# Kernel optimization log

Hardware: AMD Instinct MI355X
Metric: run time of the kernel (lower is better)

## Reference

```python
import jax, jax.numpy as jnp
import numpy as np

K = 16          # knn neighbors (init kwarg k)
GROUPS = 4      # GroupNorm groups
EPS = 1e-5
SLOPE = 0.2     # LeakyReLU negative slope


def fps(xyz, n):
    """Farthest point sampling. xyz: (B,N,3) -> idx (B,n). First index is 0 (pointnet2 convention)."""
    B, N, _ = xyz.shape

    def step(carry, _):
        dist, last = carry
        p = jnp.take_along_axis(xyz, last[:, None, None], axis=1)  # (B,1,3)
        d = jnp.sum((xyz - p) ** 2, axis=-1)                       # (B,N)
        dist = jnp.minimum(dist, d)
        nxt = jnp.argmax(dist, axis=-1).astype(jnp.int32)
        return (dist, nxt), nxt

    init = (jnp.full((B, N), jnp.inf, xyz.dtype), jnp.zeros((B,), jnp.int32))
    _, idxs = jax.lax.scan(step, init, None, length=n - 1)  # (n-1, B)
    return jnp.concatenate([jnp.zeros((B, 1), jnp.int32), idxs.T], axis=1)


def graph_feature(cq, fq, ck, fk):
    """DGCNN edge features. cq:(B,Q,3) fq:(B,Q,C) ck:(B,N,3) fk:(B,N,C) -> (B,Q,K,2C)."""
    d2 = (jnp.sum(cq * cq, -1)[:, :, None]
          - 2.0 * jnp.einsum('bqc,bnc->bqn', cq, ck)
          + jnp.sum(ck * ck, -1)[:, None, :])        # (B,Q,N)
    _, idx = jax.lax.top_k(-d2, K)                    # (B,Q,K) nearest first
    nb = jax.vmap(lambda f_, i_: f_[i_])(fk, idx)     # (B,Q,K,C)
    ctr = jnp.broadcast_to(fq[:, :, None, :], nb.shape)
    return jnp.concatenate([nb - ctr, ctr], axis=-1)


def conv_gn_lrelu(y, W, gw, gb):
    """1x1 Conv2d (no bias) + GroupNorm(4) + LeakyReLU(0.2). y: (B,Q,K,Cin), W: (Cout,Cin)."""
    y = jnp.einsum('bqkc,oc->bqko', y, W)
    B, Q, Kk, C = y.shape
    yg = y.reshape(B, Q * Kk, GROUPS, C // GROUPS)
    m = yg.mean(axis=(1, 3), keepdims=True)
    v = yg.var(axis=(1, 3), keepdims=True)
    y = ((yg - m) * jax.lax.rsqrt(v + EPS)).reshape(B, Q, Kk, C) * gw + gb
    return jnp.where(y > 0, y, SLOPE * y)


def setup_inputs() -> dict:
    key = jax.random.key(0)
    ks = jax.random.split(key, 16)
    B, N = 8, 4096
    s = lambda k_, shape, scale=0.1: (jax.random.normal(k_, shape, jnp.float32) * scale)
    return {
        'x': jax.random.normal(ks[0], (B, N, 7), jnp.float32),
        'W_in': s(ks[1], (8, 3), 0.5), 'b_in': s(ks[2], (8,), 0.02),
        'W1': s(ks[3], (32, 16), 0.2), 'g1w': jnp.ones((32,), jnp.float32), 'g1b': jnp.zeros((32,), jnp.float32),
        'W2': s(ks[4], (64, 64), 0.1), 'g2w': jnp.ones((64,), jnp.float32), 'g2b': jnp.zeros((64,), jnp.float32),
        'W3': s(ks[5], (64, 128), 0.1), 'g3w': jnp.ones((64,), jnp.float32), 'g3b': jnp.zeros((64,), jnp.float32),
        'W4': s(ks[6], (128, 128), 0.1), 'g4w': jnp.ones((128,), jnp.float32), 'g4b': jnp.zeros((128,), jnp.float32),
        'num0': 1024,
    }


def reference(x, W_in, b_in, W1, g1w, g1b, W2, g2w, g2b, W3, g3w, g3b, W4, g4w, g4b, num0):
    coor, normal, plane = x[..., :3], x[..., 3:6], x[..., 6:7]   # (B,N,3),(B,N,3),(B,N,1)

    # input_trans: Conv1d(3,8,1)
    f = jnp.einsum('bnc,oc->bno', coor, W_in) + b_in             # (B,N,8)

    g = graph_feature(coor, f, coor, f)                          # (B,N,K,16)
    f = conv_gn_lrelu(g, W1, g1w, g1b).max(axis=2)               # (B,N,32)

    idx = fps(coor, num0)
    gather = lambda a: jnp.take_along_axis(a, idx[:, :, None], axis=1)
    coor_q, normal_q, plane_q, f_q = gather(coor), gather(normal), gather(plane), gather(f)

    g = graph_feature(coor_q, f_q, coor, f)                      # (B,num0,K,64)
    f = conv_gn_lrelu(g, W2, g2w, g2b).max(axis=2)               # (B,num0,64)
    coor, normal, plane = coor_q, normal_q, plane_q

    g = graph_feature(coor, f, coor, f)                          # (B,num0,K,128)
    f = conv_gn_lrelu(g, W3, g3w, g3b).max(axis=2)               # (B,num0,64)

    idx = fps(coor, num0)  # source uses num[0] again
    gather = lambda a: jnp.take_along_axis(a, idx[:, :, None], axis=1)
    coor_q, normal_q, plane_q, f_q = gather(coor), gather(normal), gather(plane), gather(f)

    g = graph_feature(coor_q, f_q, coor, f)                      # (B,num0,K,128)
    f = conv_gn_lrelu(g, W4, g4w, g4b).max(axis=2)               # (B,num0,128)

    return coor_q, f, normal_q, plane_q
```

## Files before the change

### kernel.cpp

```cpp
#include <hip/hip_runtime.h>
#include <cstdint>

static constexpr int B   = 8;
static constexpr int N0  = 4096;
static constexpr int NQ  = 1024;
static constexpr int KNB = 16;

__device__ __forceinline__ unsigned long long wave_max_u64_l63(unsigned long long k) {
#define STEPU_(ctrl)                                                                    \
  {                                                                                     \
    unsigned lo_ = (unsigned)k, hi_ = (unsigned)(k >> 32);                              \
    unsigned plo_ = (unsigned)__builtin_amdgcn_update_dpp((int)lo_, (int)lo_, ctrl,     \
                                                          0xf, 0xf, false);             \
    unsigned phi_ = (unsigned)__builtin_amdgcn_update_dpp((int)hi_, (int)hi_, ctrl,     \
                                                          0xf, 0xf, false);             \
    unsigned long long pk_ = ((unsigned long long)phi_ << 32) | plo_;                   \
    if (pk_ > k) k = pk_;                                                               \
  }
  STEPU_(0x111) STEPU_(0x112) STEPU_(0x114) STEPU_(0x118) STEPU_(0x142) STEPU_(0x143)
#undef STEPU_
  return k;
}

__global__ void prep_kernel(const float* __restrict__ x,
                            const float* __restrict__ W_in,
                            const float* __restrict__ b_in,
                            float4* __restrict__ c4, float* __restrict__ nrm,
                            float* __restrict__ pl, float* __restrict__ f0) {
  int i = blockIdx.x * 256 + threadIdx.x;
  if (i >= B * N0) return;
  const float* xp = x + (size_t)i * 7;
  float cx = xp[0], cy = xp[1], cz = xp[2];
  float kk = __fadd_rn(__fadd_rn(__fmul_rn(cx, cx), __fmul_rn(cy, cy)), __fmul_rn(cz, cz));
  c4[i] = make_float4(cx, cy, cz, kk);
  nrm[i * 3 + 0] = xp[3]; nrm[i * 3 + 1] = xp[4]; nrm[i * 3 + 2] = xp[5];
  pl[i] = xp[6];
#pragma unroll
  for (int o = 0; o < 8; o++) {
    f0[(size_t)i * 8 + o] = cx * W_in[o * 3 + 0] + cy * W_in[o * 3 + 1] + cz * W_in[o * 3 + 2] + b_in[o];
  }
}

template <int NC>
__device__ __forceinline__ void knn_body(int bq, int lane,
                                         const float4* __restrict__ q4,
                                         const float4* __restrict__ k4,
                                         int Q, int Nk, int* __restrict__ out) {
  int b = bq / Q;
  float4 q = q4[bq];
  const float4* kb = k4 + (size_t)b * Nk + lane;
  const float INF    = __int_as_float(0x7f800000);
  const float NEGINF = __int_as_float(0xff800000);
  float myd = INF;
  int   myi = 0;
  float kth = INF;
  const bool isl0 = (lane & 15) == 0;
  constexpr int G = (NC >= 8) ? 8 : NC;
  for (int c0 = 0; c0 < NC; c0 += G) {
    float dg[G];
#pragma unroll
    for (int u = 0; u < G; u++) {
      float4 kp = kb[(c0 + u) * 64];
      float dot = __fadd_rn(__fadd_rn(__fmul_rn(q.x, kp.x), __fmul_rn(q.y, kp.y)),
                            __fmul_rn(q.z, kp.z));
      dg[u] = __fadd_rn(__fsub_rn(q.w, __fmul_rn(2.0f, dot)), kp.w);
    }
#pragma unroll
    for (int u = 0; u < G; u++) {
      float d = dg[u];
      unsigned long long m = __ballot(d < kth);
      while (m) {
        int j = __builtin_ctzll(m);
        float dv = __int_as_float(__builtin_amdgcn_readlane(__float_as_int(d), j));
        int   iv = (c0 + u) * 64 + j;
        bool gt = (myd > dv);
        float pd = __int_as_float(__builtin_amdgcn_update_dpp(
            0, __float_as_int(myd), 0x111, 0xf, 0xf, true));
        int   pi = __builtin_amdgcn_update_dpp(0, myi, 0x111, 0xf, 0xf, true);
        pd = isl0 ? NEGINF : pd;
        bool tp = (pd > dv);
        float nd = tp ? pd : dv;
        int   ni = tp ? pi : iv;
        myd = gt ? nd : myd;
        myi = gt ? ni : myi;
        kth = __int_as_float(__builtin_amdgcn_readlane(__float_as_int(myd), 15));
        m = __ballot(d < kth);
        m = (j < 63) ? (m & (~0ull << (j + 1))) : 0ull;
      }
    }
  }
  if (lane < KNB) out[(size_t)bq * KNB + lane] = myi;
}

template <int CF, int CO>
__device__ __forceinline__ void ctry_body(int i, int total, const float* __restrict__ fq,
                                          const float* __restrict__ W,
                                          float* __restrict__ ctrY,
                                          const int* __restrict__ ridx, int Q, int Nsrc) {
  if (i >= total) return;
  int o = i % CO, bq = i / CO;
  const float* fp;
  if (ridx) {
    int b = bq / Q;
    fp = fq + ((size_t)b * Nsrc + ridx[bq]) * CF;
  } else {
    fp = fq + (size_t)bq * CF;
  }
  const float* wp = W + (size_t)o * (2 * CF) + CF;
  float acc = 0.f;
#pragma unroll
  for (int c = 0; c < CF; c++) acc = fmaf(fp[c], wp[c], acc);
  ctrY[i] = acc;
}

template <int NPTS>
__device__ __forceinline__ void fps_body(const float4* __restrict__ cb, int* w) {
  constexpr int BLK = 256;
  constexpr int M = NPTS / BLK;
  constexpr int NW = BLK / 64;
  __shared__ __align__(16) float2 sxy[NPTS];
  __shared__ float szz[NPTS];
  __shared__ __align__(16) unsigned long long skey[2][NW];
  const int tid = threadIdx.x;
  const int wid = tid >> 6, lane = tid & 63;
  float cx[M], cy[M], cz[M], dist[M];
#pragma unroll
  for (int i = 0; i < M; i++) {
    float4 p = cb[tid * M + i];
    cx[i] = p.x; cy[i] = p.y; cz[i] = p.z;
    dist[i] = 3.4e38f;
    sxy[tid * M + i] = make_float2(p.x, p.y);
    szz[tid * M + i] = p.z;
  }
  w[0] = w[1] = w[2] = w[3] = 0;
  float4 p0 = cb[0];
  float px = p0.x, py = p0.y, pz = p0.z;
  __syncthreads();
  for (int t = 1; t < NQ; t++) {
    float bv = -1.f; int bi = 0;
#pragma unroll
    for (int i = 0; i < M; i++) {
      float dx = __fsub_rn(cx[i], px), dy = __fsub_rn(cy[i], py), dz = __fsub_rn(cz[i], pz);
      float d = __fadd_rn(__fadd_rn(__fmul_rn(dx, dx), __fmul_rn(dy, dy)), __fmul_rn(dz, dz));
      float dd = dist[i]; dd = (d < dd) ? d : dd; dist[i] = dd;
      if (dd > bv) { bv = dd; bi = tid * M + i; }
    }
    unsigned long long k =
        ((unsigned long long)__float_as_uint(bv) << 12) | (unsigned)(4095 - bi);
    k = wave_max_u64_l63(k);
    int p = t & 1;
    if (lane == 63) skey[p][wid] = k;
    __syncthreads();
    ulonglong2 ab = *(const ulonglong2*)&skey[p][0];
    ulonglong2 cd = *(const ulonglong2*)&skey[p][2];
    unsigned long long m0 = (ab.x > ab.y) ? ab.x : ab.y;
    unsigned long long m1 = (cd.x > cd.y) ? cd.x : cd.y;
    unsigned long long mk = (m0 > m1) ? m0 : m1;
    int win = 4095 - (int)(mk & 0xFFFull);
    float2 pxy = sxy[win];
    px = pxy.x; py = pxy.y; pz = szz[win];
    if (t == tid) w[0] = win;
    if (t == tid + 256) w[1] = win;
    if (t == tid + 512) w[2] = win;
    if (t == tid + 768) w[3] = win;
  }
}

template <int CF, int CO, int NT>
__device__ __forceinline__ void edgeconv_body(
    int blkid, const float* __restrict__ fq, const float* __restrict__ fk,
    const int* __restrict__ knn, const float* __restrict__ Wfull,
    const float* __restrict__ ctrY, const int* __restrict__ ridx,
    float* __restrict__ ymin, float* __restrict__ ymax,
    float* __restrict__ gstats, int Q, int Nk) {
  constexpr int J = CO / 4;
  constexpr int SEC = J * CF + 8;
  constexpr int NWARP = NT / 64;
  __shared__ float Wl[4 * SEC];
  __shared__ float sstat[8];
  for (int t = threadIdx.x; t < CO * CF; t += NT) {
    int o = t / CF, c = t % CF;
    Wl[(o / J) * SEC + (o % J) * CF + c] = Wfull[(size_t)o * (2 * CF) + c];
  }
  if (threadIdx.x < 8) sstat[threadIdx.x] = 0.0f;
  __syncthreads();
  const int wid = threadIdx.x >> 6, lane = threadIdx.x & 63;
  const int bq = blkid * NWARP + wid;
  const int b = bq / Q;
  const int g = lane >> 4, k = lane & 15;
  const int ni = knn[(size_t)bq * KNB + k];
  const float* nbp = fk + (size_t)(b * Nk + ni) * CF;
  const float* cp = ridx ? fq + ((size_t)b * Nk + ridx[bq]) * CF
                         : fq + (size_t)bq * CF;
  float acc[J];
#pragma unroll
  for (int j = 0; j < J; j++) acc[j] = 0.0f;
  const float* wg = &Wl[g * SEC];
#pragma unroll
  for (int c = 0; c < CF; c += 4) {
    float4 nb4 = *(const float4*)(nbp + c);
    float4 c4  = *(const float4*)(cp + c);
    float e0 = nb4.x - c4.x, e1 = nb4.y - c4.y, e2 = nb4.z - c4.z, e3 = nb4.w - c4.w;
#pragma unroll
    for (int j = 0; j < J; j++) {
      float4 w4 = *(const float4*)(wg + j * CF + c);
      acc[j] = fmaf(e0, w4.x, acc[j]);
      acc[j] = fmaf(e1, w4.y, acc[j]);
      acc[j] = fmaf(e2, w4.z, acc[j]);
      acc[j] = fmaf(e3, w4.w, acc[j]);
    }
  }
  float s = 0.f, s2 = 0.f;
  const float* cyp = ctrY + (size_t)bq * CO + g * J;
#pragma unroll
  for (int j = 0; j < J; j++) {
    float y = acc[j] + cyp[j];
    acc[j] = y;
    s += y; s2 = fmaf(y, y, s2);
  }
  float mn[J];
#pragma unroll
  for (int j = 0; j < J; j++) mn[j] = acc[j];
#pragma unroll
  for (int m = 1; m < 16; m <<= 1) {
#pragma unroll
    for (int j = 0; j < J; j++) {
      float a = __shfl_xor(acc[j], m); if (a > acc[j]) acc[j] = a;
      float c2 = __shfl_xor(mn[j], m); if (c2 < mn[j]) mn[j] = c2;
    }
    s  += __shfl_xor(s, m);
    s2 += __shfl_xor(s2, m);
  }
  if (k == 0) {
    float* mnp = ymin + (size_t)bq * CO + g * J;
    float* mxp = ymax + (size_t)bq * CO + g * J;
#pragma unroll
    for (int j = 0; j < J; j++) { mnp[j] = mn[j]; mxp[j] = acc[j]; }
    atomicAdd(&sstat[g], s);
    atomicAdd(&sstat[4 + g], s2);
  }
  __syncthreads();
  if (threadIdx.x < 8) atomicAdd(&gstats[b * 8 + threadIdx.x], sstat[threadIdx.x]);
}

__global__ __launch_bounds__(256, 2) void mega1_kernel(
    const float4* __restrict__ c40, const float* __restrict__ nrm,
    const float* __restrict__ pl, const float* __restrict__ f0,
    const float* __restrict__ W1, int* __restrict__ idx1,
    float4* __restrict__ c4q1, float* __restrict__ nq1, float* __restrict__ pq1,
    int* __restrict__ knn1, float* __restrict__ ctrY1) {
  int blk = blockIdx.x;
  if (blk < 8) {
    const int b = blk, tid = threadIdx.x;
    const float4* cb = c40 + (size_t)b * N0;
    int w[4];
    fps_body<N0>(cb, w);
    int* idxb = idx1 + (size_t)b * NQ;
#pragma unroll
    for (int u = 0; u < 4; u++) {
      int r = tid + u * 256;
      int s = (u == 0 && tid == 0) ? 0 : w[u];
      idxb[r] = s;
      c4q1[(size_t)b * NQ + r] = cb[s];
      const float* np = nrm + ((size_t)b * N0 + s) * 3;
      float* ndp = nq1 + ((size_t)b * NQ + r) * 3;
      ndp[0] = np[0]; ndp[1] = np[1]; ndp[2] = np[2];
      pq1[(size_t)b * NQ + r] = pl[(size_t)b * N0 + s];
    }
  } else if (blk < 8 + 8192) {
    int bq = (blk - 8) * 4 + (threadIdx.x >> 6);
    knn_body<64>(bq, threadIdx.x & 63, c40, c40, N0, N0, knn1);
  } else {
    int i = (blk - (8 + 8192)) * 256 + threadIdx.x;
    ctry_body<8, 32>(i, B * N0 * 32, f0, W1, ctrY1, nullptr, 0, 0);
  }
}

__global__ __launch_bounds__(256, 2) void mega2_kernel(
    const float4* __restrict__ c40, const float4* __restrict__ c4q1,
    const float* __restrict__ nq1, const float* __restrict__ pq1,
    const float* __restrict__ f0, const int* __restrict__ knn1,
    const float* __restrict__ W1, const float* __restrict__ ctrY1,
    float* __restrict__ ymin, float* __restrict__ ymax, float* __restrict__ gst1,
    int* __restrict__ idx2, float4* __restrict__ c4q2,
    float* __restrict__ cq2out, float* __restrict__ nq2out,
    float* __restrict__ pq2out, int* __restrict__ knnC, int* __restrict__ knnB) {
  int blk = blockIdx.x;
  if (blk < 8) {
    const int b = blk, tid = threadIdx.x;
    const float4* cqb = c4q1 + (size_t)b * NQ;
    int w[4];
    fps_body<NQ>(cqb, w);
    int* idxb = idx2 + (size_t)b * NQ;
#pragma unroll
    for (int u = 0; u < 4; u++) {
      int r = tid + u * 256;
      int s = (u == 0 && tid == 0) ? 0 : w[u];
      idxb[r] = s;
      float4 c = cqb[s];
      c4q2[(size_t)b * NQ + r] = c;
      float* cd = cq2out + ((size_t)b * NQ + r) * 3;
      cd[0] = c.x; cd[1] = c.y; cd[2] = c.z;
      const float* np = nq1 + ((size_t)b * NQ + s) * 3;
      float* ndp = nq2out + ((size_t)b * NQ + r) * 3;
      ndp[0] = np[0]; ndp[1] = np[1]; ndp[2] = np[2];
      pq2out[(size_t)b * NQ + r] = pq1[(size_t)b * NQ + s];
    }
  } else if (blk < 8 + 8192) {
    edgeconv_body<8, 32, 256>(blk - 8, f0, f0, knn1, W1, ctrY1, nullptr,
                              ymin, ymax, gst1, N0, N0);
  } else if (blk < 8 + 8192 + 2048) {
    int bq = (blk - (8 + 8192)) * 4 + (threadIdx.x >> 6);
    knn_body<64>(bq, threadIdx.x & 63, c4q1, c40, NQ, N0, knnC);
  } else {
    int bq = (blk - (8 + 8192 + 2048)) * 4 + (threadIdx.x >> 6);
    knn_body<16>(bq, threadIdx.x & 63, c4q1, c4q1, NQ, NQ, knnB);
  }
}

__global__ __launch_bounds__(256, 4) void mega3_kernel(
    const float4* __restrict__ c4q1, const float4* __restrict__ c4q2,
    const float* __restrict__ f3, const int* __restrict__ idx2,
    const float* __restrict__ W4, int* __restrict__ knn4, float* __restrict__ ctrY4) {
  int blk = blockIdx.x;
  if (blk < 2048) {
    int bq = blk * 4 + (threadIdx.x >> 6);
    knn_body<16>(bq, threadIdx.x & 63, c4q2, c4q1, NQ, NQ, knn4);
  } else {
    int i = (blk - 2048) * 256 + threadIdx.x;
    ctry_body<64, 128>(i, B * NQ * 128, f3, W4, ctrY4, idx2, NQ, NQ);
  }
}

template <int CF, int CO>
__global__ void ctry_kernel(const float* __restrict__ fq, const float* __restrict__ W,
                            float* __restrict__ ctrY, int total,
                            const int* __restrict__ ridx, int Q, int Nsrc) {
  int i = blockIdx.x * 256 + threadIdx.x;
  ctry_body<CF, CO>(i, total, fq, W, ctrY, ridx, Q, Nsrc);
}

template <int CF, int CO>
__global__ __launch_bounds__(256) void edgeconv_kernel(
    const float* __restrict__ fq, const float* __restrict__ fk,
    const int* __restrict__ knn, const float* __restrict__ Wfull,
    const float* __restrict__ ctrY, const int* __restrict__ ridx,
    float* __restrict__ ymin, float* __restrict__ ymax,
    float* __restrict__ gstats, int Q, int Nk) {
  edgeconv_body<CF, CO, 256>(blockIdx.x, fq, fk, knn, Wfull, ctrY, ridx,
                             ymin, ymax, gstats, Q, Nk);
}

template <int CO>
__global__ void gn_out_kernel(const float* __restrict__ ymin, const float* __restrict__ ymax,
                              const float* __restrict__ gstats, const float* __restrict__ gw,
                              const float* __restrict__ gb, float* __restrict__ fout,
                              int total, int Q, float inv_cnt) {
  int i = blockIdx.x * 256 + threadIdx.x;
  if (i >= total) return;
  constexpr int J = CO / 4;
  int o = i % CO; int bq = i / CO; int b = bq / Q;
  int g = o / J;
  float m  = gstats[b * 8 + g] * inv_cnt;
  float s2 = gstats[b * 8 + 4 + g] * inv_cnt;
  float rs = rsqrtf(s2 - m * m + 1e-5f);
  float sc = gw[o] * rs;
  float sel = (sc >= 0.f) ? ymax[i] : ymin[i];
  float v = (sel - m) * sc + gb[o];
  fout[i] = (v > 0.f) ? v : 0.2f * v;
}

extern "C" void kernel_launch(void* const* d_in, const int* in_sizes, int n_in,
                              void* d_out, int out_size, void* d_ws, size_t ws_size,
                              hipStream_t stream) {
  (void)in_sizes; (void)n_in; (void)out_size; (void)ws_size;
  const float* x    = (const float*)d_in[0];
  const float* W_in = (const float*)d_in[1];
  const float* b_in = (const float*)d_in[2];
  const float* W1   = (const float*)d_in[3];
  const float* g1w  = (const float*)d_in[4];
  const float* g1b  = (const float*)d_in[5];
  const float* W2   = (const float*)d_in[6];
  const float* g2w  = (const float*)d_in[7];
  const float* g2b  = (const float*)d_in[8];
  const float* W3   = (const float*)d_in[9];
  const float* g3w  = (const float*)d_in[10];
  const float* g3b  = (const float*)d_in[11];
  const float* W4   = (const float*)d_in[12];
  const float* g4w  = (const float*)d_in[13];
  const float* g4b  = (const float*)d_in[14];

  float* ws = (float*)d_ws;
  size_t o_c40  = 0;
  size_t o_nrm  = o_c40  + (size_t)B * N0 * 4;
  size_t o_pl   = o_nrm  + (size_t)B * N0 * 3;
  size_t o_f0   = o_pl   + (size_t)B * N0;
  size_t o_f1   = o_f0   + (size_t)B * N0 * 8;
  size_t o_ctrY = o_f1   + (size_t)B * N0 * 32;
  size_t o_ymin = o_ctrY + (size_t)B * N0 * 32;
  size_t o_ymax = o_ymin + (size_t)B * N0 * 32;
  size_t o_knnA = o_ymax + (size_t)B * N0 * 32;
  size_t o_knnB = o_knnA + (size_t)B * N0 * KNB;
  size_t o_gst  = o_knnB + (size_t)B * NQ * KNB;
  size_t o_idx1 = o_gst  + 4 * B * 8;
  size_t o_idx2 = o_idx1 + (size_t)B * NQ;
  size_t o_c4q1 = o_idx2 + (size_t)B * NQ;
  size_t o_c4q2 = o_c4q1 + (size_t)B * NQ * 4;
  size_t o_nq1  = o_c4q2 + (size_t)B * NQ * 4;
  size_t o_pq1  = o_nq1  + (size_t)B * NQ * 3;
  size_t o_f2   = o_pq1  + (size_t)B * NQ;
  size_t o_f3   = o_f2   + (size_t)B * NQ * 64;
  size_t o_knnC = o_f3   + (size_t)B * NQ * 64;

  float4* c40  = (float4*)(ws + o_c40);
  float*  nrm  = ws + o_nrm;   float* pl   = ws + o_pl;
  float*  f0   = ws + o_f0;    float* f1   = ws + o_f1;
  float*  ctrY = ws + o_ctrY;  float* ymin = ws + o_ymin;  float* ymax = ws + o_ymax;
  int*    knnA = (int*)(ws + o_knnA);
  int*    knnB = (int*)(ws + o_knnB);
  int*    knnC = (int*)(ws + o_knnC);
  float*  gst  = ws + o_gst;
  int*    idx1 = (int*)(ws + o_idx1);
  int*    idx2 = (int*)(ws + o_idx2);
  float4* c4q1 = (float4*)(ws + o_c4q1);
  float4* c4q2 = (float4*)(ws + o_c4q2);
  float*  nq1  = ws + o_nq1;   float* pq1  = ws + o_pq1;
  float*  f2   = ws + o_f2;    float* f3   = ws + o_f3;

  float* out  = (float*)d_out;
  float* cq2  = out;
  float* fout = out + (size_t)B * NQ * 3;
  float* nq2  = fout + (size_t)B * NQ * 128;
  float* pq2  = nq2 + (size_t)B * NQ * 3;

  hipMemsetAsync(gst, 0, 4 * B * 8 * sizeof(float), stream);

  prep_kernel<<<(B * N0 + 255) / 256, 256, 0, stream>>>(x, W_in, b_in, c40, nrm, pl, f0);

  mega1_kernel<<<8 + 8192 + 4096, 256, 0, stream>>>(c40, nrm, pl, f0, W1,
                                                    idx1, c4q1, nq1, pq1, knnA, ctrY);
  mega2_kernel<<<8 + 8192 + 2048 + 2048, 256, 0, stream>>>(
      c40, c4q1, nq1, pq1, f0, knnA, W1, ctrY, ymin, ymax, gst + 0,
      idx2, c4q2, cq2, nq2, pq2, knnC, knnB);
  gn_out_kernel<32><<<(B * N0 * 32 + 255) / 256, 256, 0, stream>>>(
      ymin, ymax, gst + 0, g1w, g1b, f1, B * N0 * 32, N0, 1.0f / (4096.0f * 16.0f * 8.0f));

  ctry_kernel<32, 64><<<(B * NQ * 64 + 255) / 256, 256, 0, stream>>>(
      f1, W2, ctrY, B * NQ * 64, idx1, NQ, N0);
  edgeconv_kernel<32, 64><<<B * NQ / 4, 256, 0, stream>>>(f1, f1, knnC, W2, ctrY, idx1,
                                                          ymin, ymax, gst + B * 8, NQ, N0);
  gn_out_kernel<64><<<(B * NQ * 64 + 255) / 256, 256, 0, stream>>>(
      ymin, ymax, gst + B * 8, g2w, g2b, f2, B * NQ * 64, NQ, 1.0f / (1024.0f * 16.0f * 16.0f));

  ctry_kernel<64, 64><<<(B * NQ * 64 + 255) / 256, 256, 0, stream>>>(
      f2, W3, ctrY, B * NQ * 64, nullptr, 0, 0);
  edgeconv_kernel<64, 64><<<B * NQ / 4, 256, 0, stream>>>(f2, f2, knnB, W3, ctrY, nullptr,
                                                          ymin, ymax, gst + 2 * B * 8, NQ, NQ);
  gn_out_kernel<64><<<(B * NQ * 64 + 255) / 256, 256, 0, stream>>>(
      ymin, ymax, gst + 2 * B * 8, g3w, g3b, f3, B * NQ * 64, NQ, 1.0f / (1024.0f * 16.0f * 16.0f));

  mega3_kernel<<<2048 + 4096, 256, 0, stream>>>(c4q1, c4q2, f3, idx2, W4, knnB, ctrY);
  edgeconv_kernel<64, 128><<<B * NQ / 4, 256, 0, stream>>>(f3, f3, knnB, W4, ctrY, idx2,
                                                           ymin, ymax, gst + 3 * B * 8, NQ, NQ);
  gn_out_kernel<128><<<(B * NQ * 128 + 255) / 256, 256, 0, stream>>>(
      ymin, ymax, gst + 3 * B * 8, g4w, g4b, fout, B * NQ * 128, NQ, 1.0f / (1024.0f * 16.0f * 32.0f));
}
```

Measured before the change: 1.450 ms.

## Fuse kNN selection with edge-conv so neighbor indices stay in registers

Adds a knnec_body that runs the per-query top-16 search and then goes straight into the edge-conv matmul, GN statistics and max/min reduction, using each lane's selected index from registers. The global kNN index buffers (knnA, knnC) and their separate write and read are removed. The layer-1 center projection moves into prep_kernel, and the layer-2 edge-conv now runs inside mega2 alongside FPS. The cost is fewer independent kernels to overlap, so the FPS blocks now run next to fewer kNN blocks and the mega kernels use more registers, which may lower occupancy and stretch the serial FPS critical path.

```diff
diff --git a/kernel.cpp b/kernel.cpp
--- a/kernel.cpp
+++ b/kernel.cpp
@@ -25,8 +25,10 @@
 __global__ void prep_kernel(const float* __restrict__ x,
                             const float* __restrict__ W_in,
                             const float* __restrict__ b_in,
+                            const float* __restrict__ W1,
                             float4* __restrict__ c4, float* __restrict__ nrm,
-                            float* __restrict__ pl, float* __restrict__ f0) {
+                            float* __restrict__ pl, float* __restrict__ f0,
+                            float* __restrict__ ctrY1) {
   int i = blockIdx.x * 256 + threadIdx.x;
   if (i >= B * N0) return;
   const float* xp = x + (size_t)i * 7;
@@ -35,9 +37,19 @@
   c4[i] = make_float4(cx, cy, cz, kk);
   nrm[i * 3 + 0] = xp[3]; nrm[i * 3 + 1] = xp[4]; nrm[i * 3 + 2] = xp[5];
   pl[i] = xp[6];
+  float f[8];
 #pragma unroll
   for (int o = 0; o < 8; o++) {
-    f0[(size_t)i * 8 + o] = cx * W_in[o * 3 + 0] + cy * W_in[o * 3 + 1] + cz * W_in[o * 3 + 2] + b_in[o];
+    f[o] = cx * W_in[o * 3 + 0] + cy * W_in[o * 3 + 1] + cz * W_in[o * 3 + 2] + b_in[o];
+    f0[(size_t)i * 8 + o] = f[o];
+  }
+#pragma unroll
+  for (int o = 0; o < 32; o++) {
+    const float* wp = W1 + (size_t)o * 16 + 8;
+    float acc = 0.f;
+#pragma unroll
+    for (int c = 0; c < 8; c++) acc = fmaf(f[c], wp[c], acc);
+    ctrY1[(size_t)i * 32 + o] = acc;
   }
 }
 
@@ -166,7 +178,127 @@
   }
 }
 
-template <int CF, int CO, int NT>
+template <int NC, int CF, int CO>
+__device__ __forceinline__ void knnec_body(
+    int blkid, const float4* __restrict__ q4, const float4* __restrict__ k4,
+    const float* __restrict__ fq, const float* __restrict__ fk,
+    const float* __restrict__ Wfull, const float* __restrict__ ctrY,
+    const int* __restrict__ ridx,
+    float* __restrict__ ymin, float* __restrict__ ymax,
+    float* __restrict__ gstats, int Q, int Nk) {
+  constexpr int J = CO / 4;
+  constexpr int SEC = J * CF + 8;
+  __shared__ float Wl[4 * SEC];
+  __shared__ float sstat[8];
+  for (int t = threadIdx.x; t < CO * CF; t += 256) {
+    int o = t / CF, c = t % CF;
+    Wl[(o / J) * SEC + (o % J) * CF + c] = Wfull[(size_t)o * (2 * CF) + c];
+  }
+  if (threadIdx.x < 8) sstat[threadIdx.x] = 0.0f;
+  __syncthreads();
+  const int wid = threadIdx.x >> 6, lane = threadIdx.x & 63;
+  const int bq = blkid * 4 + wid;
+  const int b = bq / Q;
+  float4 q = q4[bq];
+  const float4* kb = k4 + (size_t)b * Nk + lane;
+  const float INF    = __int_as_float(0x7f800000);
+  const float NEGINF = __int_as_float(0xff800000);
+  float myd = INF;
+  int   myi = 0;
+  float kth = INF;
+  const bool isl0 = (lane & 15) == 0;
+  constexpr int G = (NC >= 8) ? 8 : NC;
+  for (int c0 = 0; c0 < NC; c0 += G) {
+    float dg[G];
+#pragma unroll
+    for (int u = 0; u < G; u++) {
+      float4 kp = kb[(c0 + u) * 64];
+      float dot = __fadd_rn(__fadd_rn(__fmul_rn(q.x, kp.x), __fmul_rn(q.y, kp.y)),
+                            __fmul_rn(q.z, kp.z));
+      dg[u] = __fadd_rn(__fsub_rn(q.w, __fmul_rn(2.0f, dot)), kp.w);
+    }
+#pragma unroll
+    for (int u = 0; u < G; u++) {
+      float d = dg[u];
+      unsigned long long m = __ballot(d < kth);
+      while (m) {
+        int j = __builtin_ctzll(m);
+        float dv = __int_as_float(__builtin_amdgcn_readlane(__float_as_int(d), j));
+        int   iv = (c0 + u) * 64 + j;
+        bool gt = (myd > dv);
+        float pd = __int_as_float(__builtin_amdgcn_update_dpp(
+            0, __float_as_int(myd), 0x111, 0xf, 0xf, true));
+        int   pi = __builtin_amdgcn_update_dpp(0, myi, 0x111, 0xf, 0xf, true);
+        pd = isl0 ? NEGINF : pd;
+        bool tp = (pd > dv);
+        float nd = tp ? pd : dv;
+        int   nI = tp ? pi : iv;
+        myd = gt ? nd : myd;
+        myi = gt ? nI : myi;
+        kth = __int_as_float(__builtin_amdgcn_readlane(__float_as_int(myd), 15));
+        m = __ballot(d < kth);
+        m = (j < 63) ? (m & (~0ull << (j + 1))) : 0ull;
+      }
+    }
+  }
+  const int g = lane >> 4, k = lane & 15;
+  const int ni = myi;
+  (void)k;
+  const float* nbp = fk + (size_t)(b * Nk + ni) * CF;
+  const float* cp = ridx ? fq + ((size_t)b * Nk + ridx[bq]) * CF
+                         : fq + (size_t)bq * CF;
+  float acc[J];
+#pragma unroll
+  for (int j = 0; j < J; j++) acc[j] = 0.0f;
+  const float* wg = &Wl[g * SEC];
+#pragma unroll
+  for (int c = 0; c < CF; c += 4) {
+    float4 nb4 = *(const float4*)(nbp + c);
+    float4 c4  = *(const float4*)(cp + c);
+    float e0 = nb4.x - c4.x, e1 = nb4.y - c4.y, e2 = nb4.z - c4.z, e3 = nb4.w - c4.w;
+#pragma unroll
+    for (int j = 0; j < J; j++) {
+      float4 w4 = *(const float4*)(wg + j * CF + c);
+      acc[j] = fmaf(e0, w4.x, acc[j]);
+      acc[j] = fmaf(e1, w4.y, acc[j]);
+      acc[j] = fmaf(e2, w4.z, acc[j]);
+      acc[j] = fmaf(e3, w4.w, acc[j]);
+    }
+  }
+  float s = 0.f, s2 = 0.f;
+  const float* cyp = ctrY + (size_t)bq * CO + g * J;
+#pragma unroll
+  for (int j = 0; j < J; j++) {
+    float y = acc[j] + cyp[j];
+    acc[j] = y;
+    s += y; s2 = fmaf(y, y, s2);
+  }
+  float mn[J];
+#pragma unroll
+  for (int j = 0; j < J; j++) mn[j] = acc[j];
+#pragma unroll
+  for (int m = 1; m < 16; m <<= 1) {
+#pragma unroll
+    for (int j = 0; j < J; j++) {
+      float a = __shfl_xor(acc[j], m); if (a > acc[j]) acc[j] = a;
+      float c2 = __shfl_xor(mn[j], m); if (c2 < mn[j]) mn[j] = c2;
+    }
+    s  += __shfl_xor(s, m);
+    s2 += __shfl_xor(s2, m);
+  }
+  if ((lane & 15) == 0) {
+    float* mnp = ymin + (size_t)bq * CO + g * J;
+    float* mxp = ymax + (size_t)bq * CO + g * J;
+#pragma unroll
+    for (int j = 0; j < J; j++) { mnp[j] = mn[j]; mxp[j] = acc[j]; }
+    atomicAdd(&sstat[g], s);
+    atomicAdd(&sstat[4 + g], s2);
+  }
+  __syncthreads();
+  if (threadIdx.x < 8) atomicAdd(&gstats[b * 8 + threadIdx.x], sstat[threadIdx.x]);
+}
+
+template <int CF, int CO>
 __device__ __forceinline__ void edgeconv_body(
     int blkid, const float* __restrict__ fq, const float* __restrict__ fk,
     const int* __restrict__ knn, const float* __restrict__ Wfull,
@@ -175,17 +307,16 @@
     float* __restrict__ gstats, int Q, int Nk) {
   constexpr int J = CO / 4;
   constexpr int SEC = J * CF + 8;
-  constexpr int NWARP = NT / 64;
   __shared__ float Wl[4 * SEC];
   __shared__ float sstat[8];
-  for (int t = threadIdx.x; t < CO * CF; t += NT) {
+  for (int t = threadIdx.x; t < CO * CF; t += 256) {
     int o = t / CF, c = t % CF;
     Wl[(o / J) * SEC + (o % J) * CF + c] = Wfull[(size_t)o * (2 * CF) + c];
   }
   if (threadIdx.x < 8) sstat[threadIdx.x] = 0.0f;
   __syncthreads();
   const int wid = threadIdx.x >> 6, lane = threadIdx.x & 63;
-  const int bq = blkid * NWARP + wid;
+  const int bq = blkid * 4 + wid;
   const int b = bq / Q;
   const int g = lane >> 4, k = lane & 15;
   const int ni = knn[(size_t)bq * KNB + k];
@@ -246,9 +377,10 @@
 __global__ __launch_bounds__(256, 2) void mega1_kernel(
     const float4* __restrict__ c40, const float* __restrict__ nrm,
     const float* __restrict__ pl, const float* __restrict__ f0,
-    const float* __restrict__ W1, int* __restrict__ idx1,
+    const float* __restrict__ W1, const float* __restrict__ ctrY1,
+    int* __restrict__ idx1,
     float4* __restrict__ c4q1, float* __restrict__ nq1, float* __restrict__ pq1,
-    int* __restrict__ knn1, float* __restrict__ ctrY1) {
+    float* __restrict__ ymin, float* __restrict__ ymax, float* __restrict__ gst1) {
   int blk = blockIdx.x;
   if (blk < 8) {
     const int b = blk, tid = threadIdx.x;
@@ -267,24 +399,21 @@
       ndp[0] = np[0]; ndp[1] = np[1]; ndp[2] = np[2];
       pq1[(size_t)b * NQ + r] = pl[(size_t)b * N0 + s];
     }
-  } else if (blk < 8 + 8192) {
-    int bq = (blk - 8) * 4 + (threadIdx.x >> 6);
-    knn_body<64>(bq, threadIdx.x & 63, c40, c40, N0, N0, knn1);
   } else {
-    int i = (blk - (8 + 8192)) * 256 + threadIdx.x;
-    ctry_body<8, 32>(i, B * N0 * 32, f0, W1, ctrY1, nullptr, 0, 0);
+    knnec_body<64, 8, 32>(blk - 8, c40, c40, f0, f0, W1, ctrY1, nullptr,
+                          ymin, ymax, gst1, N0, N0);
   }
 }
 
 __global__ __launch_bounds__(256, 2) void mega2_kernel(
     const float4* __restrict__ c40, const float4* __restrict__ c4q1,
     const float* __restrict__ nq1, const float* __restrict__ pq1,
-    const float* __restrict__ f0, const int* __restrict__ knn1,
-    const float* __restrict__ W1, const float* __restrict__ ctrY1,
-    float* __restrict__ ymin, float* __restrict__ ymax, float* __restrict__ gst1,
+    const float* __restrict__ f1, const int* __restrict__ idx1,
+    const float* __restrict__ W2, const float* __restrict__ ctrY2,
+    float* __restrict__ ymin, float* __restrict__ ymax, float* __restrict__ gst2,
     int* __restrict__ idx2, float4* __restrict__ c4q2,
     float* __restrict__ cq2out, float* __restrict__ nq2out,
-    float* __restrict__ pq2out, int* __restrict__ knnC, int* __restrict__ knnB) {
+    float* __restrict__ pq2out, int* __restrict__ knnB) {
   int blk = blockIdx.x;
   if (blk < 8) {
     const int b = blk, tid = threadIdx.x;
@@ -306,30 +435,22 @@
       ndp[0] = np[0]; ndp[1] = np[1]; ndp[2] = np[2];
       pq2out[(size_t)b * NQ + r] = pq1[(size_t)b * NQ + s];
     }
-  } else if (blk < 8 + 8192) {
-    edgeconv_body<8, 32, 256>(blk - 8, f0, f0, knn1, W1, ctrY1, nullptr,
-                              ymin, ymax, gst1, N0, N0);
-  } else if (blk < 8 + 8192 + 2048) {
-    int bq = (blk - (8 + 8192)) * 4 + (threadIdx.x >> 6);
-    knn_body<64>(bq, threadIdx.x & 63, c4q1, c40, NQ, N0, knnC);
+  } else if (blk < 8 + 2048) {
+    knnec_body<64, 32, 64>(blk - 8, c4q1, c40, f1, f1, W2, ctrY2, idx1,
+                           ymin, ymax, gst2, NQ, N0);
   } else {
-    int bq = (blk - (8 + 8192 + 2048)) * 4 + (threadIdx.x >> 6);
+    int bq = (blk - (8 + 2048)) * 4 + (threadIdx.x >> 6);
     knn_body<16>(bq, threadIdx.x & 63, c4q1, c4q1, NQ, NQ, knnB);
   }
 }
 
-__global__ __launch_bounds__(256, 4) void mega3_kernel(
+__global__ __launch_bounds__(256) void mega3_kernel(
     const float4* __restrict__ c4q1, const float4* __restrict__ c4q2,
     const float* __restrict__ f3, const int* __restrict__ idx2,
-    const float* __restrict__ W4, int* __restrict__ knn4, float* __restrict__ ctrY4) {
-  int blk = blockIdx.x;
-  if (blk < 2048) {
-    int bq = blk * 4 + (threadIdx.x >> 6);
-    knn_body<16>(bq, threadIdx.x & 63, c4q2, c4q1, NQ, NQ, knn4);
-  } else {
-    int i = (blk - 2048) * 256 + threadIdx.x;
-    ctry_body<64, 128>(i, B * NQ * 128, f3, W4, ctrY4, idx2, NQ, NQ);
-  }
+    const float* __restrict__ W4, const float* __restrict__ ctrY4,
+    float* __restrict__ ymin, float* __restrict__ ymax, float* __restrict__ gst4) {
+  knnec_body<16, 64, 128>(blockIdx.x, c4q2, c4q1, f3, f3, W4, ctrY4, idx2,
+                          ymin, ymax, gst4, NQ, NQ);
 }
 
 template <int CF, int CO>
@@ -347,8 +468,8 @@
     const float* __restrict__ ctrY, const int* __restrict__ ridx,
     float* __restrict__ ymin, float* __restrict__ ymax,
     float* __restrict__ gstats, int Q, int Nk) {
-  edgeconv_body<CF, CO, 256>(blockIdx.x, fq, fk, knn, Wfull, ctrY, ridx,
-                             ymin, ymax, gstats, Q, Nk);
+  edgeconv_body<CF, CO>(blockIdx.x, fq, fk, knn, Wfull, ctrY, ridx,
+                        ymin, ymax, gstats, Q, Nk);
 }
 
 template <int CO>
@@ -399,8 +520,7 @@
   size_t o_ctrY = o_f1   + (size_t)B * N0 * 32;
   size_t o_ymin = o_ctrY + (size_t)B * N0 * 32;
   size_t o_ymax = o_ymin + (size_t)B * N0 * 32;
-  size_t o_knnA = o_ymax + (size_t)B * N0 * 32;
-  size_t o_knnB = o_knnA + (size_t)B * N0 * KNB;
+  size_t o_knnB = o_ymax + (size_t)B * N0 * 32;
   size_t o_gst  = o_knnB + (size_t)B * NQ * KNB;
   size_t o_idx1 = o_gst  + 4 * B * 8;
   size_t o_idx2 = o_idx1 + (size_t)B * NQ;
@@ -410,15 +530,12 @@
   size_t o_pq1  = o_nq1  + (size_t)B * NQ * 3;
   size_t o_f2   = o_pq1  + (size_t)B * NQ;
   size_t o_f3   = o_f2   + (size_t)B * NQ * 64;
-  size_t o_knnC = o_f3   + (size_t)B * NQ * 64;
 
   float4* c40  = (float4*)(ws + o_c40);
   float*  nrm  = ws + o_nrm;   float* pl   = ws + o_pl;
   float*  f0   = ws + o_f0;    float* f1   = ws + o_f1;
   float*  ctrY = ws + o_ctrY;  float* ymin = ws + o_ymin;  float* ymax = ws + o_ymax;
-  int*    knnA = (int*)(ws + o_knnA);
   int*    knnB = (int*)(ws + o_knnB);
-  int*    knnC = (int*)(ws + o_knnC);
   float*  gst  = ws + o_gst;
   int*    idx1 = (int*)(ws + o_idx1);
   int*    idx2 = (int*)(ws + o_idx2);
@@ -435,20 +552,20 @@
 
   hipMemsetAsync(gst, 0, 4 * B * 8 * sizeof(float), stream);
 
-  prep_kernel<<<(B * N0 + 255) / 256, 256, 0, stream>>>(x, W_in, b_in, c40, nrm, pl, f0);
-
-  mega1_kernel<<<8 + 8192 + 4096, 256, 0, stream>>>(c40, nrm, pl, f0, W1,
-                                                    idx1, c4q1, nq1, pq1, knnA, ctrY);
-  mega2_kernel<<<8 + 8192 + 2048 + 2048, 256, 0, stream>>>(
-      c40, c4q1, nq1, pq1, f0, knnA, W1, ctrY, ymin, ymax, gst + 0,
-      idx2, c4q2, cq2, nq2, pq2, knnC, knnB);
+  prep_kernel<<<(B * N0 + 255) / 256, 256, 0, stream>>>(x, W_in, b_in, W1,
+                                                        c40, nrm, pl, f0, ctrY);
+
+  mega1_kernel<<<8 + 8192, 256, 0, stream>>>(c40, nrm, pl, f0, W1, ctrY,
+                                             idx1, c4q1, nq1, pq1,
+                                             ymin, ymax, gst + 0);
   gn_out_kernel<32><<<(B * N0 * 32 + 255) / 256, 256, 0, stream>>>(
       ymin, ymax, gst + 0, g1w, g1b, f1, B * N0 * 32, N0, 1.0f / (4096.0f * 16.0f * 8.0f));
-
   ctry_kernel<32, 64><<<(B * NQ * 64 + 255) / 256, 256, 0, stream>>>(
       f1, W2, ctrY, B * NQ * 64, idx1, NQ, N0);
-  edgeconv_kernel<32, 64><<<B * NQ / 4, 256, 0, stream>>>(f1, f1, knnC, W2, ctrY, idx1,
-                                                          ymin, ymax, gst + B * 8, NQ, N0);
+
+  mega2_kernel<<<8 + 2048 + 2048, 256, 0, stream>>>(
+      c40, c4q1, nq1, pq1, f1, idx1, W2, ctrY, ymin, ymax, gst + B * 8,
+      idx2, c4q2, cq2, nq2, pq2, knnB);
   gn_out_kernel<64><<<(B * NQ * 64 + 255) / 256, 256, 0, stream>>>(
       ymin, ymax, gst + B * 8, g2w, g2b, f2, B * NQ * 64, NQ, 1.0f / (1024.0f * 16.0f * 16.0f));
 
@@ -459,9 +576,10 @@
   gn_out_kernel<64><<<(B * NQ * 64 + 255) / 256, 256, 0, stream>>>(
       ymin, ymax, gst + 2 * B * 8, g3w, g3b, f3, B * NQ * 64, NQ, 1.0f / (1024.0f * 16.0f * 16.0f));
 
-  mega3_kernel<<<2048 + 4096, 256, 0, stream>>>(c4q1, c4q2, f3, idx2, W4, knnB, ctrY);
-  edgeconv_kernel<64, 128><<<B * NQ / 4, 256, 0, stream>>>(f3, f3, knnB, W4, ctrY, idx2,
-                                                           ymin, ymax, gst + 3 * B * 8, NQ, NQ);
+  ctry_kernel<64, 128><<<(B * NQ * 128 + 255) / 256, 256, 0, stream>>>(
+      f3, W4, ctrY, B * NQ * 128, idx2, NQ, NQ);
+  mega3_kernel<<<B * NQ / 4, 256, 0, stream>>>(c4q1, c4q2, f3, idx2, W4, ctrY,
+                                               ymin, ymax, gst + 3 * B * 8);
   gn_out_kernel<128><<<(B * NQ * 128 + 255) / 256, 256, 0, stream>>>(
       ymin, ymax, gst + 3 * B * 8, g4w, g4b, fout, B * NQ * 128, NQ, 1.0f / (1024.0f * 16.0f * 32.0f));
 }
```

Result: no change. 1.460 ms (+0.7%).
